# Optimization experiments

Measured on AMD Instinct MI355X. Metric: run time of the kernel, lower is better.

Reference implementation:

```python
import jax, jax.numpy as jnp
import numpy as np

FS = 64.0        # BVP sampling rate (Hz)
DIST = 20        # min peak distance (samples)
FS_I = 4.0       # RR resampling rate (Hz)
NPERSEG = 256    # Welch segment length
STEP = NPERSEG // 2
_freqs = np.fft.rfftfreq(NPERSEG, 1.0 / FS_I)
_LF_IDX = np.where((_freqs >= 0.04) & (_freqs < 0.15))[0]
_HF_IDX = np.where((_freqs >= 0.15) & (_freqs < 0.4))[0]


def setup_inputs() -> dict:
    key = jax.random.key(0)
    x = jax.random.normal(key, (4096, 7680, 1), dtype=jnp.float32)
    return {"x": x}


def _mmean(v, m):
    return jnp.sum(v * m, -1) / jnp.maximum(jnp.sum(m, -1), 1.0)


def _mstd(v, m):
    mu = _mmean(v, m)
    return jnp.sqrt(jnp.maximum(_mmean((v - mu[:, None]) ** 2, m), 0.0))


def _welch(x):
    win = (0.5 - 0.5 * jnp.cos(2.0 * jnp.pi * jnp.arange(NPERSEG) / NPERSEG)).astype(x.dtype)
    scale = 1.0 / (FS_I * jnp.sum(win ** 2))
    G = x.shape[-1]
    segs = jnp.stack([x[:, s:s + NPERSEG] for s in range(0, G - NPERSEG + 1, STEP)], 1)
    segs = segs - jnp.mean(segs, -1, keepdims=True)  # detrend='constant'
    sp = jnp.fft.rfft(segs * win, axis=-1)
    p = (sp.real ** 2 + sp.imag ** 2) * scale
    p = p.at[..., 1:-1].multiply(2.0)  # one-sided (even nperseg: keep DC/Nyquist)
    return jnp.mean(p, axis=1)


def _band_trapz(psd, band_idx):
    f = jnp.asarray(_freqs[band_idx], psd.dtype)
    y = psd[:, band_idx]
    return 0.5 * jnp.sum((y[:, 1:] + y[:, :-1]) * (f[1:] - f[:-1]), -1)


def _forward(x):
    bvp = x[:, :, 0]
    B, T = bvp.shape
    K = T // DIST + 2          # max possible peaks under distance constraint
    G = int(round(T / FS * FS_I))  # 4-Hz grid length over full window

    # ---- statistical features ----
    mu = jnp.mean(bvp, -1)
    sd = jnp.std(bvp, -1)
    xc = bvp - mu[:, None]
    m2 = jnp.mean(xc ** 2, -1)
    skew = jnp.mean(xc ** 3, -1) / jnp.maximum(m2, 1e-30) ** 1.5
    kurt = jnp.mean(xc ** 4, -1) / jnp.maximum(m2, 1e-30) ** 2 - 3.0
    mn = jnp.min(bvp, -1)
    mx = jnp.max(bvp, -1)

    # ---- batched peak detection (strict local max + window-max distance suppression) ----
    is_lmax = jnp.pad((bvp[:, 1:-1] > bvp[:, :-2]) & (bvp[:, 1:-1] > bvp[:, 2:]), ((0, 0), (1, 1)))
    wmax = jax.lax.reduce_window(bvp, -jnp.inf, jax.lax.max, (1, 2 * DIST - 1), (1, 1), 'SAME')
    peak = is_lmax & (bvp >= wmax)
    ar = jnp.arange(T)
    idx = jnp.sort(jnp.where(peak, ar, T), -1)[:, :K]   # valid peak indices first, sentinel T
    valid = idx < T
    vm = valid.astype(bvp.dtype)
    npk = jnp.sum(valid, -1)
    idx_c = jnp.minimum(idx, T - 1)
    g1 = npk >= 1
    g2 = npk >= 2
    g3 = npk >= 3

    # ---- RR intervals & time-domain HRV ----
    rr = (idx[:, 1:] - idx[:, :-1]).astype(bvp.dtype) / FS   # [B, K-1]
    rr_m = vm[:, 1:]
    sdnn = jnp.where(g2, _mstd(rr, rr_m), 0.0)
    sdf = rr[:, 1:] - rr[:, :-1]
    sm = rr_m[:, 1:] * rr_m[:, :-1]
    cnt = jnp.maximum(jnp.sum(sm, -1), 1.0)
    rmssd = jnp.where(g3, jnp.sqrt(_mmean(sdf ** 2, sm)), 0.0)
    pnn50 = jnp.where(g3, jnp.sum((jnp.abs(sdf) > 0.05) * sm, -1) / cnt * 100.0, 0.0)
    sdsd = jnp.where(g3, _mstd(sdf, sm), 0.0)

    # ---- frequency-domain HRV: interp RR to 4 Hz grid, Welch PSD, LF/HF band power ----
    t_knot = jnp.concatenate([jnp.zeros((B, 1), bvp.dtype), jnp.cumsum(rr * rr_m, -1)], -1)  # [B,K]
    v_knot = jnp.concatenate([rr[:, :1], rr], -1)
    nl = jnp.clip(npk - 1, 0, K - 1)
    t_last = jnp.take_along_axis(t_knot, nl[:, None], 1)[:, 0]
    v_last = jnp.take_along_axis(v_knot, nl[:, None], 1)[:, 0]
    t_k = jnp.where(valid, t_knot, 1e9 + jnp.arange(K, dtype=bvp.dtype))  # keep xp increasing
    v_k = jnp.where(valid, v_knot, v_last[:, None])                        # hold-last extrapolation
    t_g = jnp.arange(G, dtype=bvp.dtype) / FS_I
    rr_i = jax.vmap(jnp.interp, in_axes=(None, 0, 0))(t_g, t_k, v_k)  # [B, G]
    psd = _welch(rr_i)
    cond = g3 & (t_last * FS_I > 10.0)
    lf = jnp.where(cond, _band_trapz(psd, _LF_IDX), 0.0)
    hf = jnp.where(cond, _band_trapz(psd, _HF_IDX), 0.0)
    lfhf = jnp.where(cond & (hf > 0), lf / jnp.maximum(hf, 1e-12), 0.0)

    # ---- pulse amplitude features ----
    amp = jnp.take_along_axis(bvp, idx_c, 1)
    amp_mean = jnp.where(g1, _mmean(amp, vm), 0.0)
    amp_std = jnp.where(g1, _mstd(amp, vm), 0.0)
    amp_cv = jnp.where(g1 & (amp_mean != 0), amp_std / jnp.where(amp_mean == 0, 1.0, amp_mean) * 100.0, 0.0)

    # ---- rise/fall times on first up-to-5 peaks ----
    P5 = 5
    pk5 = idx_c[:, :P5]
    jm = (jnp.arange(P5)[None, :] < jnp.minimum(npk - 1, P5)[:, None]).astype(bvp.dtype)
    offs = jnp.arange(DIST)
    gat = jax.vmap(lambda s, i: s[i])
    bi = pk5[:, :, None] - DIST + offs[None, None, :]
    bvals = jnp.where(bi >= 0, gat(bvp, jnp.clip(bi, 0, T - 1)), jnp.inf)
    rise = (DIST - jnp.argmin(bvals, -1)).astype(bvp.dtype) / FS
    fi = pk5[:, :, None] + offs[None, None, :]
    fvals = jnp.where(fi < T, gat(bvp, jnp.clip(fi, 0, T - 1)), jnp.inf)
    fall = jnp.argmin(fvals, -1).astype(bvp.dtype) / FS
    rise_t = jnp.where(g2, _mmean(rise, jm), 0.0)
    fall_t = jnp.where(g2, _mmean(fall, jm), 0.0)

    # ---- heart-rate features ----
    mean_rr = _mmean(rr, rr_m)
    mean_hr = jnp.where(g2 & (mean_rr > 0), 60.0 / jnp.maximum(mean_rr, 1e-6), 0.0)
    hr = 60.0 / jnp.maximum(rr, 1e-6)
    std_hr = jnp.where(g2, _mstd(hr, rr_m), 0.0)
    hr_rng = jnp.where(g2,
                       jnp.max(jnp.where(rr_m > 0, hr, -jnp.inf), -1) - jnp.min(jnp.where(rr_m > 0, hr, jnp.inf), -1),
                       0.0)

    f = jnp.stack([mu, sd, skew, kurt, mn, mx, mx - mn,
                   sdnn, rmssd, pnn50, sdsd,
                   lf, hf, lfhf,
                   amp_mean, amp_std, amp_cv, rise_t, fall_t,
                   mean_hr, std_hr, hr_rng, npk.astype(bvp.dtype)], -1)
    return jnp.nan_to_num(f, nan=0.0, posinf=0.0, neginf=0.0)


def reference(x):
    return _forward(x)
```

## Files before the change

### kernel.cpp

```cpp
#include <hip/hip_runtime.h>
#include <math.h>

#define TLEN 7680
#define NB 384
#define NW 6
#define CHUNK 20
#define KMAX 386

template<int CTRL>
__device__ __forceinline__ float dpp_xfer(float v){
  return __builtin_bit_cast(float, __builtin_amdgcn_update_dpp(
      0, __builtin_bit_cast(int, v), CTRL, 0xF, 0xF, true));
}
__device__ __forceinline__ float wsum(float v){
  v += dpp_xfer<0xB1>(v);
  v += dpp_xfer<0x4E>(v);
  v += dpp_xfer<0x141>(v);
  v += dpp_xfer<0x140>(v);
  v += dpp_xfer<0x142>(v);
  v += dpp_xfer<0x143>(v);
  return v;
}
__device__ __forceinline__ float wmaxr(float v){
  v = fmaxf(v, dpp_xfer<0xB1>(v));
  v = fmaxf(v, dpp_xfer<0x4E>(v));
  v = fmaxf(v, dpp_xfer<0x141>(v));
  v = fmaxf(v, dpp_xfer<0x140>(v));
  v = fmaxf(v, dpp_xfer<0x142>(v));
  v = fmaxf(v, dpp_xfer<0x143>(v));
  return v;
}
__device__ __forceinline__ float wminr(float v){
  v = fminf(v, dpp_xfer<0xB1>(v));
  v = fminf(v, dpp_xfer<0x4E>(v));
  v = fminf(v, dpp_xfer<0x141>(v));
  v = fminf(v, dpp_xfer<0x140>(v));
  v = fminf(v, dpp_xfer<0x142>(v));
  v = fminf(v, dpp_xfer<0x143>(v));
  return v;
}
__device__ __forceinline__ float hw_sin_rev(float t){
  float r; asm("v_sin_f32 %0, %1" : "=v"(r) : "v"(t)); return r;
}
__device__ __forceinline__ float hw_cos_rev(float t){
  float r; asm("v_cos_f32 %0, %1" : "=v"(r) : "v"(t)); return r;
}

__global__ __launch_bounds__(NB, 4)
void bvp_feat_kernel(const float* __restrict__ x, float* __restrict__ out){
  const int tid = threadIdx.x;
  const int lane = tid & 63;
  const int w = tid >> 6;
  const int b = blockIdx.x;

  __shared__ __align__(16) float s_bvp[TLEN];
  __shared__ __align__(16) float s_pad[CHUNK];
  __shared__ unsigned short s_pk[KMAX];
  __shared__ float s_red[17][NW];
  __shared__ int   s_wtot[NW];
  __shared__ float s_pw[46];
  __shared__ float s_rf[10];
  __shared__ float s_stash[16];
  float* const s_rri = s_bvp;
  unsigned short* const tbl = (unsigned short*)(s_bvp + 384);

  const float INVFS = 1.0f/64.0f;

  const int base = tid * CHUNK;
  if (tid < CHUNK) s_pad[tid] = -INFINITY;
  float v[CHUNK];
  float m1=0.f, m2=0.f, m3=0.f, m4=0.f, vmn=INFINITY, vmx=-INFINITY;
  {
    const float4* src4 = (const float4*)(x + (size_t)b * TLEN + base);
    float4* dst4 = (float4*)(s_bvp + base);
#pragma unroll
    for (int q = 0; q < 5; ++q){
      float4 t4 = src4[q];
      dst4[q] = t4;
      v[4*q+0]=t4.x; v[4*q+1]=t4.y; v[4*q+2]=t4.z; v[4*q+3]=t4.w;
    }
#pragma unroll
    for (int j = 0; j < CHUNK; ++j){
      float a = v[j]; float q = a*a;
      m1 += a; m2 += q; m3 += q*a; m4 += q*q;
      vmn = fminf(vmn, a); vmx = fmaxf(vmx, a);
    }
  }
  __syncthreads();

  const bool has_prev = (tid > 0);
  const bool has_next = (tid < NB-1);
  const float4* nb4 = has_next ? (const float4*)(s_bvp + base + CHUNK) : (const float4*)s_pad;
  const float4* pb4 = has_prev ? (const float4*)(s_bvp + base - CHUNK) : (const float4*)s_pad;
  const float prevs0 = has_prev ? s_bvp[base-1]     : INFINITY;
  const float next0  = has_next ? s_bvp[base+CHUNK] : INFINITY;
  const float M = vmx;

  unsigned cmask = 0u;
  {
    float pn = M;
    float4 nq;
#pragma unroll
    for (int o = 0; o < CHUNK; ++o){
      if (o >= 1){
        const int j = o - 1;
        if ((j & 3) == 0) nq = nb4[j >> 2];
        float nv = ((j&3)==0) ? nq.x : ((j&3)==1) ? nq.y : ((j&3)==2) ? nq.z : nq.w;
        pn = fmaxf(pn, nv);
      }
      float cur = v[o];
      float prevs = (o == 0) ? prevs0 : v[o-1];
      float nxts  = (o == CHUNK-1) ? next0 : v[o+1];
      if (cur > prevs && cur > nxts && cur >= pn)
        cmask |= (1u << o);
    }
  }
  unsigned pmask = 0u;
  int pcnt = 0;
  {
    float sp = -INFINITY;
    float4 pq;
#pragma unroll
    for (int o = CHUNK-1; o >= 0; --o){
      if (((cmask >> o) & 1u) && (v[o] >= sp)){ pmask |= (1u << o); ++pcnt; }
      if (o > 0){
        if ((o & 3) == 3 || o == CHUNK-1) pq = pb4[o >> 2];
        float pv = ((o&3)==0) ? pq.x : ((o&3)==1) ? pq.y : ((o&3)==2) ? pq.z : pq.w;
        sp = fmaxf(sp, pv);
      }
    }
  }

  int scan = pcnt;
#pragma unroll
  for (int off = 1; off < 64; off <<= 1){
    int t = __shfl_up(scan, off);
    if (lane >= off) scan += t;
  }
  if (lane == 63) s_wtot[w] = scan;
  __syncthreads();

  int wbase = 0, total = 0;
#pragma unroll
  for (int j = 0; j < NW; ++j){ if (j < w) wbase += s_wtot[j]; total += s_wtot[j]; }
  const int npk = total < KMAX ? total : KMAX;
  {
    float samp_p = 0.f, samp2_p = 0.f;
    int pos = wbase + scan - pcnt;
    unsigned mm = pmask;
    while (mm){
      int o = __ffs(mm) - 1;
      mm &= mm - 1u;
      if (pos < KMAX){
        s_pk[pos] = (unsigned short)(base + o);
        float a = v[o];
        samp_p += a; samp2_p += a*a;
      }
      ++pos;
    }
    m1 = wsum(m1); m2 = wsum(m2); m3 = wsum(m3); m4 = wsum(m4);
    vmn = wminr(vmn); vmx = wmaxr(vmx);
    samp_p = wsum(samp_p); samp2_p = wsum(samp2_p);
    if (lane == 63){
      s_red[9][w]=m1; s_red[10][w]=m2; s_red[11][w]=m3; s_red[12][w]=m4;
      s_red[13][w]=vmn; s_red[14][w]=vmx;
      s_red[15][w]=samp_p; s_red[16][w]=samp2_p;
    }
  }
  __syncthreads();

  const int nr = npk > 1 ? npk - 1 : 0;
  const int ns = npk > 2 ? npk - 2 : 0;
  float t_last = (npk >= 1) ? (float)((int)s_pk[npk-1]-(int)s_pk[0]) * INVFS : 0.0f;
  const bool cond = (npk >= 3) && (t_last * 4.0f > 10.0f);

  if (w == 0 || w == 2){
    float srr=0.f, srr2=0.f, shr=0.f, shr2=0.f;
    float hmx = -INFINITY, hmn = INFINITY;
    for (int i = ((w & 2) ? 64 : 0) + lane; i < nr; i += 128){
      float rr = (float)((int)s_pk[i+1]-(int)s_pk[i]) * INVFS;
      srr += rr; srr2 += rr*rr;
      float hr = 60.0f / fmaxf(rr, 1e-6f);
      shr += hr; shr2 += hr*hr;
      hmx = fmaxf(hmx, hr); hmn = fminf(hmn, hr);
    }
    srr = wsum(srr); srr2 = wsum(srr2); shr = wsum(shr); shr2 = wsum(shr2);
    hmx = wmaxr(hmx); hmn = wminr(hmn);
    if (lane == 63){
      s_red[0][w]=srr; s_red[1][w]=srr2; s_red[2][w]=shr; s_red[3][w]=shr2;
      s_red[4][w]=hmx; s_red[5][w]=hmn;
    }
  } else if (w == 1 || w == 3){
    float ssdf=0.f, ssdf2=0.f, c50=0.f;
    for (int i = ((w & 2) ? 64 : 0) + lane; i < ns; i += 128){
      float r0 = (float)((int)s_pk[i+1]-(int)s_pk[i]) * INVFS;
      float r1 = (float)((int)s_pk[i+2]-(int)s_pk[i+1]) * INVFS;
      float d = r1 - r0;
      ssdf += d; ssdf2 += d*d;
      if (fabsf(d) > 0.05f) c50 += 1.0f;
    }
    ssdf = wsum(ssdf); ssdf2 = wsum(ssdf2); c50 = wsum(c50);
    if (lane == 63){
      s_red[6][w]=ssdf; s_red[7][w]=ssdf2; s_red[8][w]=c50;
    }
  } else if (w == 4){
    if (lane < 5){
      const float* row = x + (size_t)b * TLEN;
      int limit = npk - 1;
      if (limit > 5) limit = 5;
      float rise = 0.f, fall = 0.f;
      if (lane < limit){
        int pk = (int)s_pk[lane];
        float best = INFINITY; int am = 0;
        for (int off = 0; off < 20; ++off){
          int bi = pk - 20 + off;
          float vv = (bi >= 0) ? row[bi] : INFINITY;
          if (vv < best){ best = vv; am = off; }
        }
        rise = (float)(20 - am) * INVFS;
        best = INFINITY; am = 0;
        for (int off = 0; off < 20; ++off){
          int fi = pk + off;
          float vv = (fi < TLEN) ? row[fi] : INFINITY;
          if (vv < best){ best = vv; am = off; }
        }
        fall = (float)am * INVFS;
      }
      s_rf[lane] = rise;
      s_rf[5 + lane] = fall;
    }
  } else {
    if (cond){
      const int p0 = (int)s_pk[0];
      for (int i = lane; i < npk; i += 64){
        int glo = (i == 0) ? 0 : (((int)s_pk[i] - p0 + 15) >> 4);
        int ghi = (i == npk-1) ? 383 : ((((int)s_pk[i+1] - p0 + 15) >> 4) - 1);
        if (ghi > 383) ghi = 383;
        for (int g = glo; g <= ghi; ++g) tbl[g] = (unsigned short)i;
      }
    }
  }
  __syncthreads();

  if (tid == 128){
    float M1=0.f, M2=0.f, M3=0.f, M4=0.f, MN=INFINITY, MX=-INFINITY;
    float Samp=0.f, Samp2=0.f;
#pragma unroll
    for (int j = 0; j < NW; ++j){
      M1 += s_red[9][j]; M2 += s_red[10][j]; M3 += s_red[11][j]; M4 += s_red[12][j];
      MN = fminf(MN, s_red[13][j]); MX = fmaxf(MX, s_red[14][j]);
      Samp += s_red[15][j]; Samp2 += s_red[16][j];
    }
    {
      const float invT = 1.0f / (float)TLEN;
      float mu = M1 * invT;
      float e2 = M2*invT, e3 = M3*invT, e4 = M4*invT;
      float c2 = e2 - mu*mu;
      float c3 = e3 - 3.0f*mu*e2 + 2.0f*mu*mu*mu;
      float c4 = e4 - 4.0f*mu*e3 + 6.0f*mu*mu*e2 - 3.0f*mu*mu*mu*mu;
      float m2c = fmaxf(c2, 1e-30f);
      s_stash[0] = mu;
      s_stash[1] = sqrtf(fmaxf(c2, 0.0f));
      s_stash[2] = c3 / (m2c * sqrtf(m2c));
      s_stash[3] = c4 / (m2c * m2c) - 3.0f;
      s_stash[4] = MN;
      s_stash[5] = MX;
    }
    float Srr  = s_red[0][0]+s_red[0][2], Srr2 = s_red[1][0]+s_red[1][2];
    float Shr  = s_red[2][0]+s_red[2][2], Shr2 = s_red[3][0]+s_red[3][2];
    float Hmx  = fmaxf(s_red[4][0], s_red[4][2]);
    float Hmn  = fminf(s_red[5][0], s_red[5][2]);
    float Ssdf = s_red[6][1]+s_red[6][3];
    float Ssdf2= s_red[7][1]+s_red[7][3];
    float C50  = s_red[8][1]+s_red[8][3];
    const bool g1 = npk >= 1, g2 = npk >= 2, g3 = npk >= 3;
    const float dnr = fmaxf((float)nr, 1.0f);
    const float dns = fmaxf((float)ns, 1.0f);
    const float dnp = fmaxf((float)npk, 1.0f);
    float mean_rr = Srr / dnr;
    float msdf = Ssdf / dns;
    float mhr0 = Shr / dnr;
    float amp_mean = Samp / dnp;
    float amp_std = sqrtf(fmaxf(Samp2/dnp - amp_mean*amp_mean, 0.f));
    s_stash[6]  = g2 ? sqrtf(fmaxf(Srr2/dnr - mean_rr*mean_rr, 0.f)) : 0.f;
    s_stash[7]  = g3 ? sqrtf(fmaxf(Ssdf2/dns, 0.f)) : 0.f;
    s_stash[8]  = g3 ? (C50 / dns * 100.0f) : 0.f;
    s_stash[9]  = g3 ? sqrtf(fmaxf(Ssdf2/dns - msdf*msdf, 0.f)) : 0.f;
    s_stash[10] = g1 ? amp_mean : 0.f;
    s_stash[11] = g1 ? amp_std : 0.f;
    s_stash[12] = (g1 && amp_mean != 0.f) ? amp_std / amp_mean * 100.0f : 0.f;
    s_stash[13] = (g2 && mean_rr > 0.f) ? 60.0f / fmaxf(mean_rr, 1e-6f) : 0.f;
    s_stash[14] = g2 ? sqrtf(fmaxf(Shr2/dnr - mhr0*mhr0, 0.f)) : 0.f;
    s_stash[15] = g2 ? (Hmx - Hmn) : 0.f;
  }

  if (cond){
    const int p0 = (int)s_pk[0];
    const int g = tid;
    float t = (float)g * 0.25f;
    int j = (int)tbl[g];
    float vv;
    if (j >= npk-1){
      vv = (float)((int)s_pk[npk-1]-(int)s_pk[npk-2]) * INVFS;
    } else {
      float t0 = (float)((int)s_pk[j]-p0) * INVFS;
      float t1 = (float)((int)s_pk[j+1]-p0) * INVFS;
      float v0 = (j == 0) ? (float)((int)s_pk[1]-(int)s_pk[0]) * INVFS
                          : (float)((int)s_pk[j]-(int)s_pk[j-1]) * INVFS;
      float v1 = (float)((int)s_pk[j+1]-(int)s_pk[j]) * INVFS;
      vv = v0 + (t - t0) * (v1 - v0) / (t1 - t0);
    }
    s_rri[g] = vv;
  }
  __syncthreads();

  if (cond){
    float xw0[4], xw1[4];
#pragma unroll
    for (int q = 0; q < 4; ++q){
      int n = lane + (q << 6);
      float hann = 0.5f - 0.5f * hw_cos_rev((float)n * (1.0f/256.0f));
      xw0[q] = s_rri[n]       * hann;
      xw1[q] = s_rri[128 + n] * hann;
    }
    float S0a = xw0[0]-xw0[2], S1a = xw0[1]-xw0[3], T0a = xw0[0]+xw0[2], T1a = xw0[1]+xw0[3];
    float S0b = xw1[0]-xw1[2], S1b = xw1[1]-xw1[3], T0b = xw1[0]+xw1[2], T1b = xw1[1]+xw1[3];

#define DFT_PARTIAL(K, R0, I0, R1, I1) {                                    \
      float t_ = (float)(((K) * lane) & 255) * (1.0f/256.0f);               \
      float s_ = hw_sin_rev(t_);                                            \
      float c_ = hw_cos_rev(t_);                                            \
      switch ((K) & 3){                                                     \
        case 0: { float Pa=T0a+T1a, Pb=T0b+T1b;                             \
                  R0=Pa*c_; I0=-Pa*s_; R1=Pb*c_; I1=-Pb*s_; } break;        \
        case 1: { R0 = S0a*c_ - S1a*s_; I0 = -(S0a*s_ + S1a*c_);            \
                  R1 = S0b*c_ - S1b*s_; I1 = -(S0b*s_ + S1b*c_); } break;   \
        case 2: { float Pa=T0a-T1a, Pb=T0b-T1b;                             \
                  R0=Pa*c_; I0=-Pa*s_; R1=Pb*c_; I1=-Pb*s_; } break;        \
        default:{ R0 = S0a*c_ + S1a*s_; I0 = S1a*c_ - S0a*s_;               \
                  R1 = S0b*c_ + S1b*s_; I1 = S1b*c_ - S0b*s_; } break;      \
      }                                                                     \
    }

    for (int kk = w; kk < 23; kk += 2*NW){
      const int kA = kk + 3;
      const bool hasB = (kk + NW) < 23;
      const int kB = kk + NW + 3;
      float a0,a1,a2,a3, b0=0.f,b1=0.f,b2=0.f,b3=0.f;
      DFT_PARTIAL(kA, a0, a1, a2, a3);
      if (hasB) DFT_PARTIAL(kB, b0, b1, b2, b3);
      a0 = wsum(a0); a1 = wsum(a1); a2 = wsum(a2); a3 = wsum(a3);
      b0 = wsum(b0); b1 = wsum(b1); b2 = wsum(b2); b3 = wsum(b3);
      if (lane == 63){
        s_pw[2*kk]   = (a0*a0 + a1*a1) * (2.0f/384.0f);
        s_pw[2*kk+1] = (a2*a2 + a3*a3) * (2.0f/384.0f);
        if (hasB){
          s_pw[2*(kk+NW)]   = (b0*b0 + b1*b1) * (2.0f/384.0f);
          s_pw[2*(kk+NW)+1] = (b2*b2 + b3*b3) * (2.0f/384.0f);
        }
      }
    }
#undef DFT_PARTIAL
  }
  __syncthreads();

  if (tid == 0){
    const bool g2 = npk >= 2;
    int limit = npk - 1;
    if (limit > 5) limit = 5;
    if (limit < 0) limit = 0;
    const float dlim = fmaxf((float)limit, 1.0f);
    float rise_t = g2 ? (s_rf[0]+s_rf[1]+s_rf[2]+s_rf[3]+s_rf[4]) / dlim : 0.f;
    float fall_t = g2 ? (s_rf[5]+s_rf[6]+s_rf[7]+s_rf[8]+s_rf[9]) / dlim : 0.f;
    float lf = 0.f, hf = 0.f, lfhf = 0.f;
    if (cond){
      const float df = 0.015625f;
      float acc = 0.f;
      for (int k = 3; k <= 9; ++k){
        float pk2 = 0.5f*(s_pw[2*(k-3)] + s_pw[2*(k-3)+1]);
        acc += (k == 3 || k == 9) ? 0.5f*pk2 : pk2;
      }
      lf = acc * df;
      acc = 0.f;
      for (int k = 10; k <= 25; ++k){
        float pk2 = 0.5f*(s_pw[2*(k-3)] + s_pw[2*(k-3)+1]);
        acc += (k == 10 || k == 25) ? 0.5f*pk2 : pk2;
      }
      hf = acc * df;
      if (hf > 0.f) lfhf = lf / fmaxf(hf, 1e-12f);
    }
    float feats[23] = {s_stash[0], s_stash[1], s_stash[2], s_stash[3],
                       s_stash[4], s_stash[5], s_stash[5]-s_stash[4],
                       s_stash[6], s_stash[7], s_stash[8], s_stash[9],
                       lf, hf, lfhf,
                       s_stash[10], s_stash[11], s_stash[12],
                       rise_t, fall_t,
                       s_stash[13], s_stash[14], s_stash[15], (float)npk};
    float* o = out + (size_t)b * 23;
#pragma unroll
    for (int i = 0; i < 23; ++i){
      float vv = feats[i];
      o[i] = (vv == vv && fabsf(vv) != INFINITY) ? vv : 0.0f;
    }
  }
}

extern "C" void kernel_launch(void* const* d_in, const int* in_sizes, int n_in,
                              void* d_out, int out_size, void* d_ws, size_t ws_size,
                              hipStream_t stream){
  const float* x = (const float*)d_in[0];
  float* out = (float*)d_out;
  const int B = in_sizes[0] / TLEN;
  bvp_feat_kernel<<<dim3(B), dim3(NB), 0, stream>>>(x, out);
}
```

Baseline: 74.66 us.

## Process two rows per block with software-prefetch of the next row

Each block now handles two consecutive rows. The global load of the second row is issued into registers during the first row's feature phase and written to shared memory before the final phases, so memory latency overlaps with compute. To make that possible, the RR-interpolation buffer and lookup table get their own shared arrays instead of aliasing s_bvp. The grid is halved, which costs parallelism and adds register pressure from the prefetch buffer.

```diff
diff --git a/kernel.cpp b/kernel.cpp
--- a/kernel.cpp
+++ b/kernel.cpp
@@ -47,31 +47,31 @@
 }
 
 __global__ __launch_bounds__(NB, 4)
-void bvp_feat_kernel(const float* __restrict__ x, float* __restrict__ out){
+void bvp_feat_kernel(const float* __restrict__ x, float* __restrict__ out, int B){
   const int tid = threadIdx.x;
   const int lane = tid & 63;
   const int w = tid >> 6;
-  const int b = blockIdx.x;
+  const int row0 = blockIdx.x * 2;
 
   __shared__ __align__(16) float s_bvp[TLEN];
   __shared__ __align__(16) float s_pad[CHUNK];
+  __shared__ __align__(16) float s_rri[384];
+  __shared__ unsigned short s_tbl[384];
   __shared__ unsigned short s_pk[KMAX];
   __shared__ float s_red[17][NW];
   __shared__ int   s_wtot[NW];
   __shared__ float s_pw[46];
   __shared__ float s_rf[10];
   __shared__ float s_stash[16];
-  float* const s_rri = s_bvp;
-  unsigned short* const tbl = (unsigned short*)(s_bvp + 384);
 
   const float INVFS = 1.0f/64.0f;
-
   const int base = tid * CHUNK;
   if (tid < CHUNK) s_pad[tid] = -INFINITY;
+
   float v[CHUNK];
-  float m1=0.f, m2=0.f, m3=0.f, m4=0.f, vmn=INFINITY, vmx=-INFINITY;
+  float m1=0.f,m2=0.f,m3=0.f,m4=0.f,vmn=INFINITY,vmx=-INFINITY;
   {
-    const float4* src4 = (const float4*)(x + (size_t)b * TLEN + base);
+    const float4* src4 = (const float4*)(x + (size_t)row0 * TLEN + base);
     float4* dst4 = (float4*)(s_bvp + base);
 #pragma unroll
     for (int q = 0; q < 5; ++q){
@@ -88,243 +88,271 @@
   }
   __syncthreads();
 
-  const bool has_prev = (tid > 0);
-  const bool has_next = (tid < NB-1);
-  const float4* nb4 = has_next ? (const float4*)(s_bvp + base + CHUNK) : (const float4*)s_pad;
-  const float4* pb4 = has_prev ? (const float4*)(s_bvp + base - CHUNK) : (const float4*)s_pad;
-  const float prevs0 = has_prev ? s_bvp[base-1]     : INFINITY;
-  const float next0  = has_next ? s_bvp[base+CHUNK] : INFINITY;
-  const float M = vmx;
-
-  unsigned cmask = 0u;
-  {
-    float pn = M;
-    float4 nq;
-#pragma unroll
-    for (int o = 0; o < CHUNK; ++o){
-      if (o >= 1){
-        const int j = o - 1;
-        if ((j & 3) == 0) nq = nb4[j >> 2];
-        float nv = ((j&3)==0) ? nq.x : ((j&3)==1) ? nq.y : ((j&3)==2) ? nq.z : nq.w;
-        pn = fmaxf(pn, nv);
-      }
-      float cur = v[o];
-      float prevs = (o == 0) ? prevs0 : v[o-1];
-      float nxts  = (o == CHUNK-1) ? next0 : v[o+1];
-      if (cur > prevs && cur > nxts && cur >= pn)
-        cmask |= (1u << o);
-    }
-  }
-  unsigned pmask = 0u;
-  int pcnt = 0;
-  {
-    float sp = -INFINITY;
-    float4 pq;
-#pragma unroll
-    for (int o = CHUNK-1; o >= 0; --o){
-      if (((cmask >> o) & 1u) && (v[o] >= sp)){ pmask |= (1u << o); ++pcnt; }
-      if (o > 0){
-        if ((o & 3) == 3 || o == CHUNK-1) pq = pb4[o >> 2];
-        float pv = ((o&3)==0) ? pq.x : ((o&3)==1) ? pq.y : ((o&3)==2) ? pq.z : pq.w;
-        sp = fmaxf(sp, pv);
-      }
-    }
-  }
-
-  int scan = pcnt;
-#pragma unroll
-  for (int off = 1; off < 64; off <<= 1){
-    int t = __shfl_up(scan, off);
-    if (lane >= off) scan += t;
-  }
-  if (lane == 63) s_wtot[w] = scan;
-  __syncthreads();
-
-  int wbase = 0, total = 0;
-#pragma unroll
-  for (int j = 0; j < NW; ++j){ if (j < w) wbase += s_wtot[j]; total += s_wtot[j]; }
-  const int npk = total < KMAX ? total : KMAX;
-  {
-    float samp_p = 0.f, samp2_p = 0.f;
-    int pos = wbase + scan - pcnt;
-    unsigned mm = pmask;
-    while (mm){
-      int o = __ffs(mm) - 1;
-      mm &= mm - 1u;
-      if (pos < KMAX){
-        s_pk[pos] = (unsigned short)(base + o);
-        float a = v[o];
-        samp_p += a; samp2_p += a*a;
-      }
-      ++pos;
-    }
-    m1 = wsum(m1); m2 = wsum(m2); m3 = wsum(m3); m4 = wsum(m4);
-    vmn = wminr(vmn); vmx = wmaxr(vmx);
-    samp_p = wsum(samp_p); samp2_p = wsum(samp2_p);
-    if (lane == 63){
-      s_red[9][w]=m1; s_red[10][w]=m2; s_red[11][w]=m3; s_red[12][w]=m4;
-      s_red[13][w]=vmn; s_red[14][w]=vmx;
-      s_red[15][w]=samp_p; s_red[16][w]=samp2_p;
-    }
-  }
-  __syncthreads();
-
-  const int nr = npk > 1 ? npk - 1 : 0;
-  const int ns = npk > 2 ? npk - 2 : 0;
-  float t_last = (npk >= 1) ? (float)((int)s_pk[npk-1]-(int)s_pk[0]) * INVFS : 0.0f;
-  const bool cond = (npk >= 3) && (t_last * 4.0f > 10.0f);
-
-  if (w == 0 || w == 2){
-    float srr=0.f, srr2=0.f, shr=0.f, shr2=0.f;
-    float hmx = -INFINITY, hmn = INFINITY;
-    for (int i = ((w & 2) ? 64 : 0) + lane; i < nr; i += 128){
-      float rr = (float)((int)s_pk[i+1]-(int)s_pk[i]) * INVFS;
-      srr += rr; srr2 += rr*rr;
-      float hr = 60.0f / fmaxf(rr, 1e-6f);
-      shr += hr; shr2 += hr*hr;
-      hmx = fmaxf(hmx, hr); hmn = fminf(hmn, hr);
-    }
-    srr = wsum(srr); srr2 = wsum(srr2); shr = wsum(shr); shr2 = wsum(shr2);
-    hmx = wmaxr(hmx); hmn = wminr(hmn);
-    if (lane == 63){
-      s_red[0][w]=srr; s_red[1][w]=srr2; s_red[2][w]=shr; s_red[3][w]=shr2;
-      s_red[4][w]=hmx; s_red[5][w]=hmn;
-    }
-  } else if (w == 1 || w == 3){
-    float ssdf=0.f, ssdf2=0.f, c50=0.f;
-    for (int i = ((w & 2) ? 64 : 0) + lane; i < ns; i += 128){
-      float r0 = (float)((int)s_pk[i+1]-(int)s_pk[i]) * INVFS;
-      float r1 = (float)((int)s_pk[i+2]-(int)s_pk[i+1]) * INVFS;
-      float d = r1 - r0;
-      ssdf += d; ssdf2 += d*d;
-      if (fabsf(d) > 0.05f) c50 += 1.0f;
-    }
-    ssdf = wsum(ssdf); ssdf2 = wsum(ssdf2); c50 = wsum(c50);
-    if (lane == 63){
-      s_red[6][w]=ssdf; s_red[7][w]=ssdf2; s_red[8][w]=c50;
-    }
-  } else if (w == 4){
-    if (lane < 5){
-      const float* row = x + (size_t)b * TLEN;
-      int limit = npk - 1;
-      if (limit > 5) limit = 5;
-      float rise = 0.f, fall = 0.f;
-      if (lane < limit){
-        int pk = (int)s_pk[lane];
-        float best = INFINITY; int am = 0;
-        for (int off = 0; off < 20; ++off){
-          int bi = pk - 20 + off;
-          float vv = (bi >= 0) ? row[bi] : INFINITY;
-          if (vv < best){ best = vv; am = off; }
-        }
-        rise = (float)(20 - am) * INVFS;
-        best = INFINITY; am = 0;
-        for (int off = 0; off < 20; ++off){
-          int fi = pk + off;
-          float vv = (fi < TLEN) ? row[fi] : INFINITY;
-          if (vv < best){ best = vv; am = off; }
-        }
-        fall = (float)am * INVFS;
-      }
-      s_rf[lane] = rise;
-      s_rf[5 + lane] = fall;
-    }
-  } else {
+  float4 vn4[5];
+  float n1=0.f,n2=0.f,n3=0.f,n4=0.f,nmn=INFINITY,nmx=-INFINITY;
+
+#pragma unroll
+  for (int it = 0; it < 2; ++it){
+    const int row = row0 + it;
+    if (row >= B) break;
+    const bool pre = (it == 0) && (row + 1 < B);
+
+    const bool has_prev = (tid > 0);
+    const bool has_next = (tid < NB-1);
+    const float4* nb4 = has_next ? (const float4*)(s_bvp + base + CHUNK) : (const float4*)s_pad;
+    const float4* pb4 = has_prev ? (const float4*)(s_bvp + base - CHUNK) : (const float4*)s_pad;
+    const float prevs0 = has_prev ? s_bvp[base-1]     : INFINITY;
+    const float next0  = has_next ? s_bvp[base+CHUNK] : INFINITY;
+    const float M = vmx;
+
+    unsigned cmask = 0u;
+    {
+      float pn = M;
+      float4 nq;
+#pragma unroll
+      for (int o = 0; o < CHUNK; ++o){
+        if (o >= 1){
+          const int j = o - 1;
+          if ((j & 3) == 0) nq = nb4[j >> 2];
+          float nv = ((j&3)==0) ? nq.x : ((j&3)==1) ? nq.y : ((j&3)==2) ? nq.z : nq.w;
+          pn = fmaxf(pn, nv);
+        }
+        float cur = v[o];
+        float prevs = (o == 0) ? prevs0 : v[o-1];
+        float nxts  = (o == CHUNK-1) ? next0 : v[o+1];
+        if (cur > prevs && cur > nxts && cur >= pn)
+          cmask |= (1u << o);
+      }
+    }
+    unsigned pmask = 0u;
+    int pcnt = 0;
+    {
+      float sp = -INFINITY;
+      float4 pq;
+#pragma unroll
+      for (int o = CHUNK-1; o >= 0; --o){
+        if (((cmask >> o) & 1u) && (v[o] >= sp)){ pmask |= (1u << o); ++pcnt; }
+        if (o > 0){
+          if ((o & 3) == 3 || o == CHUNK-1) pq = pb4[o >> 2];
+          float pv = ((o&3)==0) ? pq.x : ((o&3)==1) ? pq.y : ((o&3)==2) ? pq.z : pq.w;
+          sp = fmaxf(sp, pv);
+        }
+      }
+    }
+
+    int scan = pcnt;
+#pragma unroll
+    for (int off = 1; off < 64; off <<= 1){
+      int t = __shfl_up(scan, off);
+      if (lane >= off) scan += t;
+    }
+    if (lane == 63) s_wtot[w] = scan;
+    __syncthreads();
+
+    int wbase = 0, total = 0;
+#pragma unroll
+    for (int j = 0; j < NW; ++j){ if (j < w) wbase += s_wtot[j]; total += s_wtot[j]; }
+    const int npk = total < KMAX ? total : KMAX;
+    {
+      float samp_p = 0.f, samp2_p = 0.f;
+      int pos = wbase + scan - pcnt;
+      unsigned mm = pmask;
+      while (mm){
+        int o = __ffs(mm) - 1;
+        mm &= mm - 1u;
+        if (pos < KMAX){
+          s_pk[pos] = (unsigned short)(base + o);
+          float a = v[o];
+          samp_p += a; samp2_p += a*a;
+        }
+        ++pos;
+      }
+      m1 = wsum(m1); m2 = wsum(m2); m3 = wsum(m3); m4 = wsum(m4);
+      vmn = wminr(vmn); vmx = wmaxr(vmx);
+      samp_p = wsum(samp_p); samp2_p = wsum(samp2_p);
+      if (lane == 63){
+        s_red[9][w]=m1; s_red[10][w]=m2; s_red[11][w]=m3; s_red[12][w]=m4;
+        s_red[13][w]=vmn; s_red[14][w]=vmx;
+        s_red[15][w]=samp_p; s_red[16][w]=samp2_p;
+      }
+    }
+    __syncthreads();
+
+    const int nr = npk > 1 ? npk - 1 : 0;
+    const int ns = npk > 2 ? npk - 2 : 0;
+    float t_last = (npk >= 1) ? (float)((int)s_pk[npk-1]-(int)s_pk[0]) * INVFS : 0.0f;
+    const bool cond = (npk >= 3) && (t_last * 4.0f > 10.0f);
+
+    if (pre){
+      const float4* nsrc = (const float4*)(x + (size_t)(row+1) * TLEN + base);
+#pragma unroll
+      for (int q = 0; q < 5; ++q) vn4[q] = nsrc[q];
+    }
+
+    if (w == 0 || w == 2){
+      float srr=0.f, srr2=0.f, shr=0.f, shr2=0.f;
+      float hmx = -INFINITY, hmn = INFINITY;
+      for (int i = ((w & 2) ? 64 : 0) + lane; i < nr; i += 128){
+        float rr = (float)((int)s_pk[i+1]-(int)s_pk[i]) * INVFS;
+        srr += rr; srr2 += rr*rr;
+        float hr = 60.0f / fmaxf(rr, 1e-6f);
+        shr += hr; shr2 += hr*hr;
+        hmx = fmaxf(hmx, hr); hmn = fminf(hmn, hr);
+      }
+      srr = wsum(srr); srr2 = wsum(srr2); shr = wsum(shr); shr2 = wsum(shr2);
+      hmx = wmaxr(hmx); hmn = wminr(hmn);
+      if (lane == 63){
+        s_red[0][w]=srr; s_red[1][w]=srr2; s_red[2][w]=shr; s_red[3][w]=shr2;
+        s_red[4][w]=hmx; s_red[5][w]=hmn;
+      }
+    } else if (w == 1 || w == 3){
+      float ssdf=0.f, ssdf2=0.f, c50=0.f;
+      for (int i = ((w & 2) ? 64 : 0) + lane; i < ns; i += 128){
+        float r0 = (float)((int)s_pk[i+1]-(int)s_pk[i]) * INVFS;
+        float r1 = (float)((int)s_pk[i+2]-(int)s_pk[i+1]) * INVFS;
+        float d = r1 - r0;
+        ssdf += d; ssdf2 += d*d;
+        if (fabsf(d) > 0.05f) c50 += 1.0f;
+      }
+      ssdf = wsum(ssdf); ssdf2 = wsum(ssdf2); c50 = wsum(c50);
+      if (lane == 63){
+        s_red[6][w]=ssdf; s_red[7][w]=ssdf2; s_red[8][w]=c50;
+      }
+    } else if (w == 4){
+      if (lane < 5){
+        const float* rowp = x + (size_t)row * TLEN;
+        int limit = npk - 1;
+        if (limit > 5) limit = 5;
+        float rise = 0.f, fall = 0.f;
+        if (lane < limit){
+          int pk = (int)s_pk[lane];
+          float best = INFINITY; int am = 0;
+          for (int off = 0; off < 20; ++off){
+            int bi = pk - 20 + off;
+            float vv = (bi >= 0) ? rowp[bi] : INFINITY;
+            if (vv < best){ best = vv; am = off; }
+          }
+          rise = (float)(20 - am) * INVFS;
+          best = INFINITY; am = 0;
+          for (int off = 0; off < 20; ++off){
+            int fi = pk + off;
+            float vv = (fi < TLEN) ? rowp[fi] : INFINITY;
+            if (vv < best){ best = vv; am = off; }
+          }
+          fall = (float)am * INVFS;
+        }
+        s_rf[lane] = rise;
+        s_rf[5 + lane] = fall;
+      }
+    } else {
+      if (cond){
+        const int p0 = (int)s_pk[0];
+        for (int i = lane; i < npk; i += 64){
+          int glo = (i == 0) ? 0 : (((int)s_pk[i] - p0 + 15) >> 4);
+          int ghi = (i == npk-1) ? 383 : ((((int)s_pk[i+1] - p0 + 15) >> 4) - 1);
+          if (ghi > 383) ghi = 383;
+          for (int g = glo; g <= ghi; ++g) s_tbl[g] = (unsigned short)i;
+        }
+      }
+    }
+
+    if (pre){
+      float4* dst4 = (float4*)(s_bvp + base);
+      n1=0.f; n2=0.f; n3=0.f; n4=0.f; nmn=INFINITY; nmx=-INFINITY;
+#pragma unroll
+      for (int q = 0; q < 5; ++q){
+        float4 t4 = vn4[q];
+        dst4[q] = t4;
+#define NACC(a) { float _a=(a); n1+=_a; float _q=_a*_a; n2+=_q; n3+=_q*_a; n4+=_q*_q; nmn=fminf(nmn,_a); nmx=fmaxf(nmx,_a); }
+        NACC(t4.x) NACC(t4.y) NACC(t4.z) NACC(t4.w)
+#undef NACC
+      }
+    }
+    __syncthreads();
+
+    if (tid == 128){
+      float M1=0.f, M2=0.f, M3=0.f, M4=0.f, MN=INFINITY, MX=-INFINITY;
+      float Samp=0.f, Samp2=0.f;
+#pragma unroll
+      for (int j = 0; j < NW; ++j){
+        M1 += s_red[9][j]; M2 += s_red[10][j]; M3 += s_red[11][j]; M4 += s_red[12][j];
+        MN = fminf(MN, s_red[13][j]); MX = fmaxf(MX, s_red[14][j]);
+        Samp += s_red[15][j]; Samp2 += s_red[16][j];
+      }
+      {
+        const float invT = 1.0f / (float)TLEN;
+        float mu = M1 * invT;
+        float e2 = M2*invT, e3 = M3*invT, e4 = M4*invT;
+        float c2 = e2 - mu*mu;
+        float c3 = e3 - 3.0f*mu*e2 + 2.0f*mu*mu*mu;
+        float c4 = e4 - 4.0f*mu*e3 + 6.0f*mu*mu*e2 - 3.0f*mu*mu*mu*mu;
+        float m2c = fmaxf(c2, 1e-30f);
+        s_stash[0] = mu;
+        s_stash[1] = sqrtf(fmaxf(c2, 0.0f));
+        s_stash[2] = c3 / (m2c * sqrtf(m2c));
+        s_stash[3] = c4 / (m2c * m2c) - 3.0f;
+        s_stash[4] = MN;
+        s_stash[5] = MX;
+      }
+      float Srr  = s_red[0][0]+s_red[0][2], Srr2 = s_red[1][0]+s_red[1][2];
+      float Shr  = s_red[2][0]+s_red[2][2], Shr2 = s_red[3][0]+s_red[3][2];
+      float Hmx  = fmaxf(s_red[4][0], s_red[4][2]);
+      float Hmn  = fminf(s_red[5][0], s_red[5][2]);
+      float Ssdf = s_red[6][1]+s_red[6][3];
+      float Ssdf2= s_red[7][1]+s_red[7][3];
+      float C50  = s_red[8][1]+s_red[8][3];
+      const bool g1 = npk >= 1, g2 = npk >= 2, g3 = npk >= 3;
+      const float dnr = fmaxf((float)nr, 1.0f);
+      const float dns = fmaxf((float)ns, 1.0f);
+      const float dnp = fmaxf((float)npk, 1.0f);
+      float mean_rr = Srr / dnr;
+      float msdf = Ssdf / dns;
+      float mhr0 = Shr / dnr;
+      float amp_mean = Samp / dnp;
+      float amp_std = sqrtf(fmaxf(Samp2/dnp - amp_mean*amp_mean, 0.f));
+      s_stash[6]  = g2 ? sqrtf(fmaxf(Srr2/dnr - mean_rr*mean_rr, 0.f)) : 0.f;
+      s_stash[7]  = g3 ? sqrtf(fmaxf(Ssdf2/dns, 0.f)) : 0.f;
+      s_stash[8]  = g3 ? (C50 / dns * 100.0f) : 0.f;
+      s_stash[9]  = g3 ? sqrtf(fmaxf(Ssdf2/dns - msdf*msdf, 0.f)) : 0.f;
+      s_stash[10] = g1 ? amp_mean : 0.f;
+      s_stash[11] = g1 ? amp_std : 0.f;
+      s_stash[12] = (g1 && amp_mean != 0.f) ? amp_std / amp_mean * 100.0f : 0.f;
+      s_stash[13] = (g2 && mean_rr > 0.f) ? 60.0f / fmaxf(mean_rr, 1e-6f) : 0.f;
+      s_stash[14] = g2 ? sqrtf(fmaxf(Shr2/dnr - mhr0*mhr0, 0.f)) : 0.f;
+      s_stash[15] = g2 ? (Hmx - Hmn) : 0.f;
+    }
+
     if (cond){
       const int p0 = (int)s_pk[0];
-      for (int i = lane; i < npk; i += 64){
-        int glo = (i == 0) ? 0 : (((int)s_pk[i] - p0 + 15) >> 4);
-        int ghi = (i == npk-1) ? 383 : ((((int)s_pk[i+1] - p0 + 15) >> 4) - 1);
-        if (ghi > 383) ghi = 383;
-        for (int g = glo; g <= ghi; ++g) tbl[g] = (unsigned short)i;
-      }
-    }
-  }
-  __syncthreads();
-
-  if (tid == 128){
-    float M1=0.f, M2=0.f, M3=0.f, M4=0.f, MN=INFINITY, MX=-INFINITY;
-    float Samp=0.f, Samp2=0.f;
-#pragma unroll
-    for (int j = 0; j < NW; ++j){
-      M1 += s_red[9][j]; M2 += s_red[10][j]; M3 += s_red[11][j]; M4 += s_red[12][j];
-      MN = fminf(MN, s_red[13][j]); MX = fmaxf(MX, s_red[14][j]);
-      Samp += s_red[15][j]; Samp2 += s_red[16][j];
-    }
-    {
-      const float invT = 1.0f / (float)TLEN;
-      float mu = M1 * invT;
-      float e2 = M2*invT, e3 = M3*invT, e4 = M4*invT;
-      float c2 = e2 - mu*mu;
-      float c3 = e3 - 3.0f*mu*e2 + 2.0f*mu*mu*mu;
-      float c4 = e4 - 4.0f*mu*e3 + 6.0f*mu*mu*e2 - 3.0f*mu*mu*mu*mu;
-      float m2c = fmaxf(c2, 1e-30f);
-      s_stash[0] = mu;
-      s_stash[1] = sqrtf(fmaxf(c2, 0.0f));
-      s_stash[2] = c3 / (m2c * sqrtf(m2c));
-      s_stash[3] = c4 / (m2c * m2c) - 3.0f;
-      s_stash[4] = MN;
-      s_stash[5] = MX;
-    }
-    float Srr  = s_red[0][0]+s_red[0][2], Srr2 = s_red[1][0]+s_red[1][2];
-    float Shr  = s_red[2][0]+s_red[2][2], Shr2 = s_red[3][0]+s_red[3][2];
-    float Hmx  = fmaxf(s_red[4][0], s_red[4][2]);
-    float Hmn  = fminf(s_red[5][0], s_red[5][2]);
-    float Ssdf = s_red[6][1]+s_red[6][3];
-    float Ssdf2= s_red[7][1]+s_red[7][3];
-    float C50  = s_red[8][1]+s_red[8][3];
-    const bool g1 = npk >= 1, g2 = npk >= 2, g3 = npk >= 3;
-    const float dnr = fmaxf((float)nr, 1.0f);
-    const float dns = fmaxf((float)ns, 1.0f);
-    const float dnp = fmaxf((float)npk, 1.0f);
-    float mean_rr = Srr / dnr;
-    float msdf = Ssdf / dns;
-    float mhr0 = Shr / dnr;
-    float amp_mean = Samp / dnp;
-    float amp_std = sqrtf(fmaxf(Samp2/dnp - amp_mean*amp_mean, 0.f));
-    s_stash[6]  = g2 ? sqrtf(fmaxf(Srr2/dnr - mean_rr*mean_rr, 0.f)) : 0.f;
-    s_stash[7]  = g3 ? sqrtf(fmaxf(Ssdf2/dns, 0.f)) : 0.f;
-    s_stash[8]  = g3 ? (C50 / dns * 100.0f) : 0.f;
-    s_stash[9]  = g3 ? sqrtf(fmaxf(Ssdf2/dns - msdf*msdf, 0.f)) : 0.f;
-    s_stash[10] = g1 ? amp_mean : 0.f;
-    s_stash[11] = g1 ? amp_std : 0.f;
-    s_stash[12] = (g1 && amp_mean != 0.f) ? amp_std / amp_mean * 100.0f : 0.f;
-    s_stash[13] = (g2 && mean_rr > 0.f) ? 60.0f / fmaxf(mean_rr, 1e-6f) : 0.f;
-    s_stash[14] = g2 ? sqrtf(fmaxf(Shr2/dnr - mhr0*mhr0, 0.f)) : 0.f;
-    s_stash[15] = g2 ? (Hmx - Hmn) : 0.f;
-  }
-
-  if (cond){
-    const int p0 = (int)s_pk[0];
-    const int g = tid;
-    float t = (float)g * 0.25f;
-    int j = (int)tbl[g];
-    float vv;
-    if (j >= npk-1){
-      vv = (float)((int)s_pk[npk-1]-(int)s_pk[npk-2]) * INVFS;
-    } else {
-      float t0 = (float)((int)s_pk[j]-p0) * INVFS;
-      float t1 = (float)((int)s_pk[j+1]-p0) * INVFS;
-      float v0 = (j == 0) ? (float)((int)s_pk[1]-(int)s_pk[0]) * INVFS
-                          : (float)((int)s_pk[j]-(int)s_pk[j-1]) * INVFS;
-      float v1 = (float)((int)s_pk[j+1]-(int)s_pk[j]) * INVFS;
-      vv = v0 + (t - t0) * (v1 - v0) / (t1 - t0);
-    }
-    s_rri[g] = vv;
-  }
-  __syncthreads();
-
-  if (cond){
-    float xw0[4], xw1[4];
-#pragma unroll
-    for (int q = 0; q < 4; ++q){
-      int n = lane + (q << 6);
-      float hann = 0.5f - 0.5f * hw_cos_rev((float)n * (1.0f/256.0f));
-      xw0[q] = s_rri[n]       * hann;
-      xw1[q] = s_rri[128 + n] * hann;
-    }
-    float S0a = xw0[0]-xw0[2], S1a = xw0[1]-xw0[3], T0a = xw0[0]+xw0[2], T1a = xw0[1]+xw0[3];
-    float S0b = xw1[0]-xw1[2], S1b = xw1[1]-xw1[3], T0b = xw1[0]+xw1[2], T1b = xw1[1]+xw1[3];
+      const int g = tid;
+      float t = (float)g * 0.25f;
+      int j = (int)s_tbl[g];
+      float vv;
+      if (j >= npk-1){
+        vv = (float)((int)s_pk[npk-1]-(int)s_pk[npk-2]) * INVFS;
+      } else {
+        float t0 = (float)((int)s_pk[j]-p0) * INVFS;
+        float t1 = (float)((int)s_pk[j+1]-p0) * INVFS;
+        float v0 = (j == 0) ? (float)((int)s_pk[1]-(int)s_pk[0]) * INVFS
+                            : (float)((int)s_pk[j]-(int)s_pk[j-1]) * INVFS;
+        float v1 = (float)((int)s_pk[j+1]-(int)s_pk[j]) * INVFS;
+        vv = v0 + (t - t0) * (v1 - v0) / (t1 - t0);
+      }
+      s_rri[g] = vv;
+    }
+    __syncthreads();
+
+    if (cond){
+      float xw0[4], xw1[4];
+#pragma unroll
+      for (int q = 0; q < 4; ++q){
+        int n = lane + (q << 6);
+        float hann = 0.5f - 0.5f * hw_cos_rev((float)n * (1.0f/256.0f));
+        xw0[q] = s_rri[n]       * hann;
+        xw1[q] = s_rri[128 + n] * hann;
+      }
+      float S0a = xw0[0]-xw0[2], S1a = xw0[1]-xw0[3], T0a = xw0[0]+xw0[2], T1a = xw0[1]+xw0[3];
+      float S0b = xw1[0]-xw1[2], S1b = xw1[1]-xw1[3], T0b = xw1[0]+xw1[2], T1b = xw1[1]+xw1[3];
 
 #define DFT_PARTIAL(K, R0, I0, R1, I1) {                                    \
       float t_ = (float)(((K) * lane) & 255) * (1.0f/256.0f);               \
@@ -342,65 +370,74 @@
       }                                                                     \
     }
 
-    for (int kk = w; kk < 23; kk += 2*NW){
-      const int kA = kk + 3;
-      const bool hasB = (kk + NW) < 23;
-      const int kB = kk + NW + 3;
-      float a0,a1,a2,a3, b0=0.f,b1=0.f,b2=0.f,b3=0.f;
-      DFT_PARTIAL(kA, a0, a1, a2, a3);
-      if (hasB) DFT_PARTIAL(kB, b0, b1, b2, b3);
-      a0 = wsum(a0); a1 = wsum(a1); a2 = wsum(a2); a3 = wsum(a3);
-      b0 = wsum(b0); b1 = wsum(b1); b2 = wsum(b2); b3 = wsum(b3);
-      if (lane == 63){
-        s_pw[2*kk]   = (a0*a0 + a1*a1) * (2.0f/384.0f);
-        s_pw[2*kk+1] = (a2*a2 + a3*a3) * (2.0f/384.0f);
-        if (hasB){
-          s_pw[2*(kk+NW)]   = (b0*b0 + b1*b1) * (2.0f/384.0f);
-          s_pw[2*(kk+NW)+1] = (b2*b2 + b3*b3) * (2.0f/384.0f);
-        }
-      }
-    }
+      for (int kk = w; kk < 23; kk += 2*NW){
+        const int kA = kk + 3;
+        const bool hasB = (kk + NW) < 23;
+        const int kB = kk + NW + 3;
+        float a0,a1,a2,a3, b0=0.f,b1=0.f,b2=0.f,b3=0.f;
+        DFT_PARTIAL(kA, a0, a1, a2, a3);
+        if (hasB) DFT_PARTIAL(kB, b0, b1, b2, b3);
+        a0 = wsum(a0); a1 = wsum(a1); a2 = wsum(a2); a3 = wsum(a3);
+        b0 = wsum(b0); b1 = wsum(b1); b2 = wsum(b2); b3 = wsum(b3);
+        if (lane == 63){
+          s_pw[2*kk]   = (a0*a0 + a1*a1) * (2.0f/384.0f);
+          s_pw[2*kk+1] = (a2*a2 + a3*a3) * (2.0f/384.0f);
+          if (hasB){
+            s_pw[2*(kk+NW)]   = (b0*b0 + b1*b1) * (2.0f/384.0f);
+            s_pw[2*(kk+NW)+1] = (b2*b2 + b3*b3) * (2.0f/384.0f);
+          }
+        }
+      }
 #undef DFT_PARTIAL
-  }
-  __syncthreads();
-
-  if (tid == 0){
-    const bool g2 = npk >= 2;
-    int limit = npk - 1;
-    if (limit > 5) limit = 5;
-    if (limit < 0) limit = 0;
-    const float dlim = fmaxf((float)limit, 1.0f);
-    float rise_t = g2 ? (s_rf[0]+s_rf[1]+s_rf[2]+s_rf[3]+s_rf[4]) / dlim : 0.f;
-    float fall_t = g2 ? (s_rf[5]+s_rf[6]+s_rf[7]+s_rf[8]+s_rf[9]) / dlim : 0.f;
-    float lf = 0.f, hf = 0.f, lfhf = 0.f;
-    if (cond){
-      const float df = 0.015625f;
-      float acc = 0.f;
-      for (int k = 3; k <= 9; ++k){
-        float pk2 = 0.5f*(s_pw[2*(k-3)] + s_pw[2*(k-3)+1]);
-        acc += (k == 3 || k == 9) ? 0.5f*pk2 : pk2;
-      }
-      lf = acc * df;
-      acc = 0.f;
-      for (int k = 10; k <= 25; ++k){
-        float pk2 = 0.5f*(s_pw[2*(k-3)] + s_pw[2*(k-3)+1]);
-        acc += (k == 10 || k == 25) ? 0.5f*pk2 : pk2;
-      }
-      hf = acc * df;
-      if (hf > 0.f) lfhf = lf / fmaxf(hf, 1e-12f);
-    }
-    float feats[23] = {s_stash[0], s_stash[1], s_stash[2], s_stash[3],
-                       s_stash[4], s_stash[5], s_stash[5]-s_stash[4],
-                       s_stash[6], s_stash[7], s_stash[8], s_stash[9],
-                       lf, hf, lfhf,
-                       s_stash[10], s_stash[11], s_stash[12],
-                       rise_t, fall_t,
-                       s_stash[13], s_stash[14], s_stash[15], (float)npk};
-    float* o = out + (size_t)b * 23;
-#pragma unroll
-    for (int i = 0; i < 23; ++i){
-      float vv = feats[i];
-      o[i] = (vv == vv && fabsf(vv) != INFINITY) ? vv : 0.0f;
+    }
+    __syncthreads();
+
+    if (tid == 0){
+      const bool g2 = npk >= 2;
+      int limit = npk - 1;
+      if (limit > 5) limit = 5;
+      if (limit < 0) limit = 0;
+      const float dlim = fmaxf((float)limit, 1.0f);
+      float rise_t = g2 ? (s_rf[0]+s_rf[1]+s_rf[2]+s_rf[3]+s_rf[4]) / dlim : 0.f;
+      float fall_t = g2 ? (s_rf[5]+s_rf[6]+s_rf[7]+s_rf[8]+s_rf[9]) / dlim : 0.f;
+      float lf = 0.f, hf = 0.f, lfhf = 0.f;
+      if (cond){
+        const float df = 0.015625f;
+        float acc = 0.f;
+        for (int k = 3; k <= 9; ++k){
+          float pk2 = 0.5f*(s_pw[2*(k-3)] + s_pw[2*(k-3)+1]);
+          acc += (k == 3 || k == 9) ? 0.5f*pk2 : pk2;
+        }
+        lf = acc * df;
+        acc = 0.f;
+        for (int k = 10; k <= 25; ++k){
+          float pk2 = 0.5f*(s_pw[2*(k-3)] + s_pw[2*(k-3)+1]);
+          acc += (k == 10 || k == 25) ? 0.5f*pk2 : pk2;
+        }
+        hf = acc * df;
+        if (hf > 0.f) lfhf = lf / fmaxf(hf, 1e-12f);
+      }
+      float feats[23] = {s_stash[0], s_stash[1], s_stash[2], s_stash[3],
+                         s_stash[4], s_stash[5], s_stash[5]-s_stash[4],
+                         s_stash[6], s_stash[7], s_stash[8], s_stash[9],
+                         lf, hf, lfhf,
+                         s_stash[10], s_stash[11], s_stash[12],
+                         rise_t, fall_t,
+                         s_stash[13], s_stash[14], s_stash[15], (float)npk};
+      float* o = out + (size_t)row * 23;
+#pragma unroll
+      for (int i = 0; i < 23; ++i){
+        float vv = feats[i];
+        o[i] = (vv == vv && fabsf(vv) != INFINITY) ? vv : 0.0f;
+      }
+    }
+
+    if (pre){
+#pragma unroll
+      for (int q = 0; q < 5; ++q){
+        v[4*q+0]=vn4[q].x; v[4*q+1]=vn4[q].y; v[4*q+2]=vn4[q].z; v[4*q+3]=vn4[q].w;
+      }
+      m1=n1; m2=n2; m3=n3; m4=n4; vmn=nmn; vmx=nmx;
     }
   }
 }
@@ -411,5 +448,6 @@
   const float* x = (const float*)d_in[0];
   float* out = (float*)d_out;
   const int B = in_sizes[0] / TLEN;
-  bvp_feat_kernel<<<dim3(B), dim3(NB), 0, stream>>>(x, out);
-}
+  const int G = (B + 1) / 2;
+  bvp_feat_kernel<<<dim3(G), dim3(NB), 0, stream>>>(x, out, B);
+}
```

New measurement: 101.0 us. 1.35x slower.
